# Kernel tuning notes

Measured on AMD Instinct MI355X. Metric: run time of the kernel, lower is better.

The kernel has to match this reference:

```python
import jax, jax.numpy as jnp
import numpy as np

B, M, GRID = 4, 8192, 32          # batches, points per batch, voxel grid side
N = B * M
K = 8                              # knn neighbors (includes self at dist 0)
C_IN, C_OUT, H = 8, 8, 128
KEYB = 64                          # hash base (coords shifted +1 stay in [0,33])
EPS = 1e-5


def setup_inputs() -> dict:
    rng = np.random.default_rng(0)
    # unique occupied voxels per batch (ME SparseTensor requires unique coords)
    cs = []
    for b in range(B):
        lin = rng.choice(GRID ** 3, size=M, replace=False)
        x, y, z = lin // (GRID * GRID), (lin // GRID) % GRID, lin % GRID
        cs.append(np.stack([np.full(M, b), x, y, z], axis=1))
    coords = jnp.asarray(np.concatenate(cs, axis=0).astype(np.int32))  # [N,4]

    key = jax.random.key(0)
    ks = jax.random.split(key, 4)
    feats = jax.random.normal(ks[0], (N, C_IN), jnp.float32)
    w1 = jax.random.normal(ks[1], ((K + 1) * C_IN, H), jnp.float32) * 0.05  # 1x1 conv
    g1 = jnp.ones((H,), jnp.float32)
    b1 = jnp.zeros((H,), jnp.float32)
    w3 = jax.random.normal(ks[2], (27, H, H), jnp.float32) * 0.02          # 3^3 sparse conv
    g2 = jnp.ones((H,), jnp.float32)
    b2 = jnp.zeros((H,), jnp.float32)
    w_out = jax.random.normal(ks[3], (H, 2 * C_OUT), jnp.float32) * 0.05   # 1x1 conv
    return dict(coords=coords, feats=feats, w1=w1, g1=g1, b1=b1,
                w3=w3, g2=g2, b2=b2, w_out=w_out)


def _knn_idx(coords):
    # per-batch brute-force kNN on xyz (batch column segments the search)
    xyz = coords[:, 1:].astype(jnp.float32).reshape(B, M, 3)
    d2 = jnp.sum((xyz[:, :, None, :] - xyz[:, None, :, :]) ** 2, -1)  # [B,M,M]
    _, idx = jax.lax.top_k(-d2, K)                                     # [B,M,K]
    return (idx + (jnp.arange(B) * M)[:, None, None]).reshape(N, K)


def _bn(x, g, b):
    mu = jnp.mean(x, axis=0)
    var = jnp.var(x, axis=0)
    return (x - mu) * jax.lax.rsqrt(var + EPS) * g + b


def reference(coords, feats, w1, g1, b1, w3, g2, b2, w_out):
    # --- kNN gather-and-build: [center || k neighbor feats] -> (k+1)*C_in ---
    nbr = _knn_idx(coords)                                        # [N,K] int
    combined = jnp.concatenate([feats[:, None, :], feats[nbr]], axis=1)
    combined = combined.reshape(N, (K + 1) * C_IN)
    # --- neighbor_processor: 1x1 conv + BN + ReLU ---
    h = jax.nn.relu(_bn(combined @ w1, g1, b1))                   # [N,H]
    # --- context_predictor conv k=3: gather inputs at coord+offset via hash ---
    c = coords[:, 1:] + 1                                         # shift so offsets stay >= 0
    keys = ((coords[:, 0] * KEYB + c[:, 0]) * KEYB + c[:, 1]) * KEYB + c[:, 2]
    order = jnp.argsort(keys)
    skeys = keys[order]
    offs = jnp.stack(jnp.meshgrid(*([jnp.arange(-1, 2)] * 3), indexing='ij'),
                     axis=-1).reshape(27, 3)                      # {-1,0,1}^3
    okey = (offs[:, 0] * KEYB + offs[:, 1]) * KEYB + offs[:, 2]   # [27]
    q = keys[None, :] + okey[:, None]                             # [27,N]
    pos = jnp.clip(jnp.searchsorted(skeys, q), 0, N - 1)
    valid = skeys[pos] == q                                       # [27,N]
    j = order[pos]                                                # [27,N]
    gathered = jnp.where(valid[..., None], h[j], 0.0)             # [27,N,H]
    h2 = jnp.einsum('onc,ocd->nd', gathered, w3)                  # [N,H]
    h2 = jax.nn.relu(_bn(h2, g2, b2))
    # --- final 1x1 conv -> mean/scale ---
    return h2 @ w_out                                             # [N, 2*C_OUT]
```

## Files before the change

### kernel.cpp

```cpp
#include <hip/hip_runtime.h>
#include <hip/hip_bf16.h>

#define B_   4
#define M_   8192
#define N_   32768
#define H_   128
#define EPS_ 1e-5f
#define TBL  1048576
#define GUARD 8192

typedef short short8 __attribute__((ext_vector_type(8)));
typedef float f32x4  __attribute__((ext_vector_type(4)));

__global__ __launch_bounds__(256) void prep_pack_kernel(const int* __restrict__ coords,
                                                        int* __restrict__ table,
                                                        int* __restrict__ packed,
                                                        int* __restrict__ keyb,
                                                        const float* __restrict__ w3,
                                                        ushort* __restrict__ w3f,
                                                        float* __restrict__ gsum1,
                                                        float* __restrict__ gsum2,
                                                        unsigned int* __restrict__ hbz) {
    int bid = blockIdx.x, tid = threadIdx.x;
    if (bid < 128) {
        int n = bid * 256 + tid;
        int b = coords[4*n+0], x = coords[4*n+1], y = coords[4*n+2], z = coords[4*n+3];
        packed[n] = (x << 10) | (y << 5) | z;
        int key = ((b*64 + x+1)*64 + y+1)*64 + (z+1);
        keyb[n] = key;
        table[key] = n;
        if (bid < 8)  gsum1[bid*256 + tid] = 0.f;
        if (bid == 0) gsum2[tid] = 0.f;
        if (bid == 8 && tid < 64) hbz[tid] = 0u;
        return;
    }
    int t = (bid - 128) * 256 + tid;
    int lane = t & 63;
    int ct   = (t >> 6) & 7;
    int ks   = (t >> 9) & 3;
    int o    = t >> 11;
    int quad = lane >> 4, l15 = lane & 15;
    int n = ct*16 + l15;
    const float* src = w3 + o*16384;
    ushort out8[8];
#pragma unroll
    for (int j = 0; j < 8; ++j) {
        int c = ks*32 + quad*8 + j;
        float v = src[c*128 + n];
        __hip_bfloat16 bv = __float2bfloat16(v);
        ushort u; __builtin_memcpy(&u, &bv, 2);
        out8[j] = u;
    }
    *(uint4*)&w3f[t*8] = *(uint4*)out8;
}

__global__ __launch_bounds__(256) void knn_kernel(const int* __restrict__ table,
                                                  const int* __restrict__ keyb,
                                                  const int* __restrict__ packed,
                                                  int* __restrict__ nbr) {
    __shared__ int okey_sh[96], d2_sh[96];
    __shared__ int tops[256 * 8];
    __shared__ int flagq[32];
    __shared__ int ncnt, fln;
    int tid = threadIdx.x;
    if (tid == 0) { ncnt = 0; fln = 0; }
    __syncthreads();
    if (tid < 125) {
        int dx = tid / 25 - 2, rr = tid % 25, dy = rr / 5 - 2, dz = rr % 5 - 2;
        int d2 = dx*dx + dy*dy + dz*dz;
        if (d2 <= 8) {
            int p = atomicAdd(&ncnt, 1);
            okey_sh[p] = dx * 4096 + dy * 64 + dz;
            d2_sh[p]   = d2;
        }
    }
    __syncthreads();
    if (tid < 3) { okey_sh[93 + tid] = 0; d2_sh[93 + tid] = 9; }
    __syncthreads();

    int qloc = tid >> 3;
    int q    = blockIdx.x * 32 + qloc;
    int sub  = tid & 7;
    int kb   = keyb[q];

    int top[8];
#pragma unroll
    for (int k = 0; k < 8; ++k) top[k] = 0x7FFFFFFF;

    int base = sub * 12;
    for (int i = 0; i < 12; ++i) {
        int idx = base + i;
        int j = table[kb + okey_sh[idx]];
        if (j >= 0) {
            int key = (d2_sh[idx] << 13) | (j & 8191);
            if (key < top[7]) {
#pragma unroll
                for (int k = 7; k >= 1; --k)
                    top[k] = (key < top[k]) ? max(key, top[k-1]) : top[k];
                top[0] = min(key, top[0]);
            }
        }
    }
#pragma unroll
    for (int k = 0; k < 8; ++k) tops[tid*8 + k] = top[k];
    __syncthreads();

    if (sub == 0) {
        const int* L = &tops[tid*8];
        int ia0=0, ia1=0, ia2=0, ia3=0, ia4=0, ia5=0, ia6=0, ia7=0;
        int res[8];
#pragma unroll
        for (int k = 0; k < 8; ++k) {
            int v0 = L[ia0],      v1 = L[8 + ia1],  v2 = L[16 + ia2], v3 = L[24 + ia3];
            int v4 = L[32 + ia4], v5 = L[40 + ia5], v6 = L[48 + ia6], v7 = L[56 + ia7];
            int m01 = min(v0, v1), m23 = min(v2, v3);
            int m45 = min(v4, v5), m67 = min(v6, v7);
            int m = min(min(m01, m23), min(m45, m67));
            res[k] = m;
            if      (m == v0) ++ia0; else if (m == v1) ++ia1;
            else if (m == v2) ++ia2; else if (m == v3) ++ia3;
            else if (m == v4) ++ia4; else if (m == v5) ++ia5;
            else if (m == v6) ++ia6; else ++ia7;
        }
        int bb = q & ~(M_-1);
        if ((res[7] >> 13) <= 8) {
#pragma unroll
            for (int k = 0; k < 8; ++k) nbr[q*8 + k] = bb + (res[k] & 8191);
        } else {
            int pos = atomicAdd(&fln, 1);
            flagq[pos] = q;
        }
    }
    __syncthreads();

    int fcnt = fln;
    for (int f = 0; f < fcnt; ++f) {
        int n = flagq[f];
        int bb = n & ~(M_-1);
        int p = packed[n];
        int qx = (p >> 10) & 31, qy = (p >> 5) & 31, qz = p & 31;
        int bt[8];
#pragma unroll
        for (int k = 0; k < 8; ++k) bt[k] = 0x7FFFFFFF;
        for (int j = tid; j < M_; j += 256) {
            int c = packed[bb + j];
            int dx = qx - ((c >> 10) & 31);
            int dy = qy - ((c >> 5) & 31);
            int dz = qz - (c & 31);
            int d2 = dx*dx + dy*dy + dz*dz;
            int key = (d2 << 13) | j;
            if (key < bt[7]) {
#pragma unroll
                for (int k = 7; k >= 1; --k)
                    bt[k] = (key < bt[k]) ? max(key, bt[k-1]) : bt[k];
                bt[0] = min(key, bt[0]);
            }
        }
#pragma unroll
        for (int k = 0; k < 8; ++k) tops[tid*8 + k] = bt[k];
        __syncthreads();
        for (int stride = 128; stride >= 1; stride >>= 1) {
            if (tid < stride) {
                int* A  = &tops[tid*8];
                int* Bp = &tops[(tid+stride)*8];
                int r[8]; int ia = 0, ib = 0;
#pragma unroll
                for (int k = 0; k < 8; ++k) {
                    int a = A[ia], b2 = Bp[ib];
                    if (a <= b2) { r[k] = a; ++ia; } else { r[k] = b2; ++ib; }
                }
#pragma unroll
                for (int k = 0; k < 8; ++k) A[k] = r[k];
            }
            __syncthreads();
        }
        if (tid == 0) {
#pragma unroll
            for (int k = 0; k < 8; ++k) nbr[n*8 + k] = bb + (tops[k] & 8191);
        }
        __syncthreads();
    }
}

__global__ __launch_bounds__(256) void h1_kernel(const float* __restrict__ feats,
                                                 const int* __restrict__ nbr,
                                                 const float* __restrict__ w1,
                                                 float* __restrict__ hpre,
                                                 float* __restrict__ gsum1) {
    __shared__ float comb[16][72];
    __shared__ float ssum[256], ssq[256];
    int tid = threadIdx.x;
    int rowbase = blockIdx.x * 16;
    if (tid < 144) {
        int r = tid / 9, s = tid % 9;
        int grow = rowbase + r;
        int idx = (s == 0) ? grow : nbr[grow*8 + (s-1)];
        const float4* f = (const float4*)(feats + idx * 8);
        float4 a = f[0], b = f[1];
        float* dp = &comb[r][s*8];
        dp[0]=a.x; dp[1]=a.y; dp[2]=a.z; dp[3]=a.w;
        dp[4]=b.x; dp[5]=b.y; dp[6]=b.z; dp[7]=b.w;
    }
    __syncthreads();
    int c = tid & 127, rh = tid >> 7;
    float acc[8];
#pragma unroll
    for (int i = 0; i < 8; ++i) acc[i] = 0.f;
    for (int s = 0; s < 72; ++s) {
        float w = w1[s*128 + c];
#pragma unroll
        for (int i = 0; i < 8; ++i)
            acc[i] += comb[rh*8 + i][s] * w;
    }
    float s = 0.f, q = 0.f;
#pragma unroll
    for (int i = 0; i < 8; ++i) {
        hpre[(rowbase + rh*8 + i)*128 + c] = acc[i];
        s += acc[i]; q += acc[i]*acc[i];
    }
    ssum[tid] = s; ssq[tid] = q;
    __syncthreads();
    if (tid < 128) {
        float S = ssum[tid] + ssum[tid+128];
        float Q = ssq[tid]  + ssq[tid+128];
        float* g = gsum1 + (blockIdx.x & 7) * 256;
        atomicAdd(&g[tid], S);
        atomicAdd(&g[128 + tid], Q);
    }
}

__global__ __launch_bounds__(256) void bnrelu_bf16_kernel(const float* __restrict__ x,
                                                          const float* __restrict__ gsum1,
                                                          const float* __restrict__ g1,
                                                          const float* __restrict__ b1,
                                                          ushort* __restrict__ y) {
    __shared__ float sc[128], sh[128];
    int tid = threadIdx.x;
    if (tid < 128) {
        float s = 0.f, q = 0.f;
#pragma unroll
        for (int r = 0; r < 8; ++r) {
            s += gsum1[r*256 + tid];
            q += gsum1[r*256 + 128 + tid];
        }
        float mu  = s / (float)N_;
        float var = q / (float)N_ - mu*mu;
        float inv = rsqrtf(var + EPS_);
        float scv = inv * g1[tid];
        sc[tid] = scv;
        sh[tid] = b1[tid] - mu * scv;
    }
    __syncthreads();
    int i = blockIdx.x * 256 + tid;
    float4 v = ((const float4*)x)[i];
    int c = (i * 4) & 127;
    v.x = fmaxf(0.f, v.x*sc[c]   + sh[c]);
    v.y = fmaxf(0.f, v.y*sc[c+1] + sh[c+1]);
    v.z = fmaxf(0.f, v.z*sc[c+2] + sh[c+2]);
    v.w = fmaxf(0.f, v.w*sc[c+3] + sh[c+3]);
    ushort o[4];
#pragma unroll
    for (int k = 0; k < 4; ++k) {
        float f = (&v.x)[k];
        __hip_bfloat16 bv = __float2bfloat16(f);
        __builtin_memcpy(&o[k], &bv, 2);
    }
    ((ushort4*)y)[i] = make_ushort4(o[0], o[1], o[2], o[3]);
}

#define CONV3_LDS 145408
__global__ __launch_bounds__(512) void conv3_mfma_kernel(const ushort* __restrict__ hb,
                                                         const ushort* __restrict__ w3f,
                                                         const int* __restrict__ table,
                                                         const int* __restrict__ keyb,
                                                         float* __restrict__ h2,
                                                         float* __restrict__ gsum) {
    extern __shared__ char smem_raw[];
    ushort* Asb = (ushort*)smem_raw;
    ushort* Bsb = (ushort*)(smem_raw + 65536);
    int*    jsh = (int*)(smem_raw + 131072);
    int*    kbsh= (int*)(smem_raw + 144896);

    int tid = threadIdx.x;
    int lane = tid & 63, wid = tid >> 6;
    int quad = lane >> 4, l15 = lane & 15;
    int bid = blockIdx.x;
    int swz = (bid & 7) * 32 + (bid >> 3);
    int rowbase = swz * 128;
    int wr = wid >> 1;
    int cb = (wid & 1) * 4;

    if (tid < 128) kbsh[tid] = keyb[rowbase + tid];
    __syncthreads();
    for (int t = tid; t < 27*128; t += 512) {
        int o = t >> 7, r = t & 127;
        int dx = o/9 - 1, dy = (o/3)%3 - 1, dz = o%3 - 1;
        jsh[t] = table[kbsh[r] + dx*4096 + dy*64 + dz];
    }
    __syncthreads();

#pragma unroll
    for (int i = 0; i < 4; ++i) {
        int flat = i*512 + tid;
        int r = flat >> 4, cp = flat & 15;
        int j = jsh[r];
        const ushort* asrc = hb + j*128 + ((cp ^ (r & 15)) << 3);
        __builtin_amdgcn_global_load_lds(
            (const __attribute__((address_space(1))) unsigned int*)asrc,
            (__attribute__((address_space(3))) unsigned int*)&Asb[flat << 3],
            16, 0, 0);
        __builtin_amdgcn_global_load_lds(
            (const __attribute__((address_space(1))) unsigned int*)(w3f + (flat << 3)),
            (__attribute__((address_space(3))) unsigned int*)&Bsb[flat << 3],
            16, 0, 0);
    }
    __syncthreads();

    f32x4 acc[2][4];
#pragma unroll
    for (int i = 0; i < 2; ++i)
#pragma unroll
        for (int c = 0; c < 4; ++c)
            acc[i][c] = (f32x4){0.f, 0.f, 0.f, 0.f};

    int cur = 0;
#pragma unroll 1
    for (int o = 0; o < 27; ++o) {
        if (o < 26) {
            int obase = (o + 1) << 7;
            const ushort* wsrc = w3f + ((o + 1) << 14);
            int dst = (cur ^ 1) * 16384;
#pragma unroll
            for (int i = 0; i < 4; ++i) {
                int flat = i*512 + tid;
                int r = flat >> 4, cp = flat & 15;
                int j = jsh[obase + r];
                const ushort* asrc = hb + j*128 + ((cp ^ (r & 15)) << 3);
                __builtin_amdgcn_global_load_lds(
                    (const __attribute__((address_space(1))) unsigned int*)asrc,
                    (__attribute__((address_space(3))) unsigned int*)&Asb[dst + (flat << 3)],
                    16, 0, 0);
                __builtin_amdgcn_global_load_lds(
                    (const __attribute__((address_space(1))) unsigned int*)(wsrc + (flat << 3)),
                    (__attribute__((address_space(3))) unsigned int*)&Bsb[dst + (flat << 3)],
                    16, 0, 0);
            }
        }
        const ushort* Ac = Asb + cur*16384;
        const ushort* Bc = Bsb + cur*16384;
#pragma unroll
        for (int ks = 0; ks < 4; ++ks) {
            short8 af[2], bfr[4];
#pragma unroll
            for (int i = 0; i < 2; ++i) {
                int lr = wr*32 + i*16 + l15;
                int chunk = (ks*4 + quad) ^ l15;
                af[i] = *(const short8*)&Ac[lr*128 + chunk*8];
            }
#pragma unroll
            for (int c = 0; c < 4; ++c)
                bfr[c] = *(const short8*)&Bc[((ks*8 + cb + c)*64 + lane) << 3];
#pragma unroll
            for (int i = 0; i < 2; ++i)
#pragma unroll
                for (int c = 0; c < 4; ++c)
                    acc[i][c] = __builtin_amdgcn_mfma_f32_16x16x32_bf16(af[i], bfr[c], acc[i][c], 0, 0, 0);
        }
        __syncthreads();
        cur ^= 1;
    }

    float s[4], q[4];
#pragma unroll
    for (int c = 0; c < 4; ++c) { s[c] = 0.f; q[c] = 0.f; }
#pragma unroll
    for (int i = 0; i < 2; ++i)
#pragma unroll
        for (int c = 0; c < 4; ++c)
#pragma unroll
            for (int r = 0; r < 4; ++r) {
                int row = rowbase + wr*32 + i*16 + quad*4 + r;
                int col = (cb + c)*16 + l15;
                float v = acc[i][c][r];
                h2[row*128 + col] = v;
                s[c] += v; q[c] += v*v;
            }
    float* red = (float*)smem_raw;
    if (tid < 256) red[tid] = 0.f;
    __syncthreads();
#pragma unroll
    for (int c = 0; c < 4; ++c) {
        int col = (cb + c)*16 + l15;
        atomicAdd(&red[col], s[c]);
        atomicAdd(&red[128 + col], q[c]);
    }
    __syncthreads();
    if (tid < 256) atomicAdd(&gsum[tid], red[tid]);
}

__global__ __launch_bounds__(256) void out_kernel(const float* __restrict__ h2,
                                                  const float* __restrict__ wout,
                                                  const float* __restrict__ gsum2,
                                                  const float* __restrict__ g2,
                                                  const float* __restrict__ b2,
                                                  float* __restrict__ out) {
    __shared__ float hrow[128][129];
    __shared__ float wsh[2048];
    __shared__ float sc[128], sh[128];
    int tid = threadIdx.x;
    if (tid < 128) {
        float s = gsum2[tid], q = gsum2[128 + tid];
        float mu  = s / (float)N_;
        float var = q / (float)N_ - mu*mu;
        float inv = rsqrtf(var + EPS_);
        float scv = inv * g2[tid];
        sc[tid] = scv;
        sh[tid] = b2[tid] - mu * scv;
    }
#pragma unroll
    for (int i = 0; i < 8; ++i) wsh[i*256 + tid] = wout[i*256 + tid];
    __syncthreads();

    int rowbase = blockIdx.x * 128;
#pragma unroll
    for (int i = 0; i < 16; ++i) {
        int flat = i*256 + tid;
        int row = flat >> 5, c4 = (flat & 31) * 4;
        float4 v = *(const float4*)&h2[(rowbase + row)*128 + c4];
        float4 scv = *(const float4*)&sc[c4];
        float4 shv = *(const float4*)&sh[c4];
        hrow[row][c4+0] = fmaxf(0.f, fmaf(v.x, scv.x, shv.x));
        hrow[row][c4+1] = fmaxf(0.f, fmaf(v.y, scv.y, shv.y));
        hrow[row][c4+2] = fmaxf(0.f, fmaf(v.z, scv.z, shv.z));
        hrow[row][c4+3] = fmaxf(0.f, fmaf(v.w, scv.w, shv.w));
    }
    __syncthreads();

    int row = tid >> 1, dbase = (tid & 1) * 8;
    float acc[8];
#pragma unroll
    for (int k = 0; k < 8; ++k) acc[k] = 0.f;
    for (int c = 0; c < 128; ++c) {
        float hv = hrow[row][c];
        float4 w0 = *(const float4*)&wsh[c*16 + dbase];
        float4 w1 = *(const float4*)&wsh[c*16 + dbase + 4];
        acc[0] = fmaf(hv, w0.x, acc[0]);
        acc[1] = fmaf(hv, w0.y, acc[1]);
        acc[2] = fmaf(hv, w0.z, acc[2]);
        acc[3] = fmaf(hv, w0.w, acc[3]);
        acc[4] = fmaf(hv, w1.x, acc[4]);
        acc[5] = fmaf(hv, w1.y, acc[5]);
        acc[6] = fmaf(hv, w1.z, acc[6]);
        acc[7] = fmaf(hv, w1.w, acc[7]);
    }
    float* op = out + (rowbase + row)*16 + dbase;
    *(float4*)op       = (float4){acc[0], acc[1], acc[2], acc[3]};
    *(float4*)(op + 4) = (float4){acc[4], acc[5], acc[6], acc[7]};
}

extern "C" void kernel_launch(void* const* d_in, const int* in_sizes, int n_in,
                              void* d_out, int out_size, void* d_ws, size_t ws_size,
                              hipStream_t stream) {
    const int*   coords = (const int*)d_in[0];
    const float* feats  = (const float*)d_in[1];
    const float* w1     = (const float*)d_in[2];
    const float* g1     = (const float*)d_in[3];
    const float* b1     = (const float*)d_in[4];
    const float* w3     = (const float*)d_in[5];
    const float* g2     = (const float*)d_in[6];
    const float* b2     = (const float*)d_in[7];
    const float* wout   = (const float*)d_in[8];
    float* out = (float*)d_out;

    char* ws = (char*)d_ws;
    int*    table_base = (int*)(ws);
    int*    table   = table_base + GUARD;
    int*    packed  = (int*)(ws + (4352u<<10));
    int*    keyb    = (int*)(ws + (4608u<<10));
    int*    nbr     = (int*)(ws + (4864u<<10));
    float*  gsum2   = (float*)(ws + (6416u<<10));
    float*  gsum1   = (float*)(ws + (6420u<<10));
    ushort* w3f     = (ushort*)(ws + (6656u<<10));
    ushort* hb      = (ushort*)(ws + (7680u<<10));
    float*  h       = (float*)(ws + (15872u<<10));
    float*  h2      = h;

    static bool conv3_attr_set = false;
    if (!conv3_attr_set) {
        hipFuncSetAttribute(reinterpret_cast<const void*>(&conv3_mfma_kernel),
                            hipFuncAttributeMaxDynamicSharedMemorySize, CONV3_LDS);
        conv3_attr_set = true;
    }

    hipMemsetAsync(table_base, 0xFF, (TBL + GUARD) * sizeof(int), stream);
    prep_pack_kernel <<<344, 256, 0, stream>>>(coords, table, packed, keyb, w3, w3f,
                                               gsum1, gsum2, (unsigned int*)(hb - 128));
    knn_kernel       <<<N_/32, 256, 0, stream>>>(table, keyb, packed, nbr);
    h1_kernel        <<<N_/16, 256, 0, stream>>>(feats, nbr, w1, h, gsum1);
    bnrelu_bf16_kernel<<<(N_*H_/4)/256, 256, 0, stream>>>(h, gsum1, g1, b1, hb);
    conv3_mfma_kernel<<<N_/128, 512, CONV3_LDS, stream>>>(hb, w3f, table, keyb, h2, gsum2);
    out_kernel       <<<N_/128, 256, 0, stream>>>(h2, wout, gsum2, g2, b2, out);
}
```

Before: 213.9 us.

## Assign one wavefront per kNN query with shuffle-based top-8 selection

The kNN kernel now maps each query to a full 64-lane wavefront. Each lane probes one or two of the 93 hash offsets, and the 8 smallest keys are picked by repeated wave-wide xor-shuffle min reductions. This replaces the per-thread insertion sort, the LDS staging and the serial 8-way merge. The grid grows from N/32 to N/4 blocks, and each block still pays the offset-table setup and still reserves the 8 KB tops array for the rare brute-force fallback, which may limit occupancy.

```diff
diff --git a/kernel.cpp b/kernel.cpp
--- a/kernel.cpp
+++ b/kernel.cpp
@@ -58,9 +58,9 @@
                                                   const int* __restrict__ keyb,
                                                   const int* __restrict__ packed,
                                                   int* __restrict__ nbr) {
-    __shared__ int okey_sh[96], d2_sh[96];
+    __shared__ int okey_sh[93], d2_sh[93];
     __shared__ int tops[256 * 8];
-    __shared__ int flagq[32];
+    __shared__ int flagq[4];
     __shared__ int ncnt, fln;
     int tid = threadIdx.x;
     if (tid == 0) { ncnt = 0; fln = 0; }
@@ -75,54 +75,37 @@
         }
     }
     __syncthreads();
-    if (tid < 3) { okey_sh[93 + tid] = 0; d2_sh[93 + tid] = 9; }
-    __syncthreads();
-
-    int qloc = tid >> 3;
-    int q    = blockIdx.x * 32 + qloc;
-    int sub  = tid & 7;
-    int kb   = keyb[q];
-
-    int top[8];
-#pragma unroll
-    for (int k = 0; k < 8; ++k) top[k] = 0x7FFFFFFF;
-
-    int base = sub * 12;
-    for (int i = 0; i < 12; ++i) {
-        int idx = base + i;
-        int j = table[kb + okey_sh[idx]];
-        if (j >= 0) {
-            int key = (d2_sh[idx] << 13) | (j & 8191);
-            if (key < top[7]) {
-#pragma unroll
-                for (int k = 7; k >= 1; --k)
-                    top[k] = (key < top[k]) ? max(key, top[k-1]) : top[k];
-                top[0] = min(key, top[0]);
-            }
-        }
-    }
-#pragma unroll
-    for (int k = 0; k < 8; ++k) tops[tid*8 + k] = top[k];
-    __syncthreads();
-
-    if (sub == 0) {
-        const int* L = &tops[tid*8];
-        int ia0=0, ia1=0, ia2=0, ia3=0, ia4=0, ia5=0, ia6=0, ia7=0;
-        int res[8];
-#pragma unroll
-        for (int k = 0; k < 8; ++k) {
-            int v0 = L[ia0],      v1 = L[8 + ia1],  v2 = L[16 + ia2], v3 = L[24 + ia3];
-            int v4 = L[32 + ia4], v5 = L[40 + ia5], v6 = L[48 + ia6], v7 = L[56 + ia7];
-            int m01 = min(v0, v1), m23 = min(v2, v3);
-            int m45 = min(v4, v5), m67 = min(v6, v7);
-            int m = min(min(m01, m23), min(m45, m67));
-            res[k] = m;
-            if      (m == v0) ++ia0; else if (m == v1) ++ia1;
-            else if (m == v2) ++ia2; else if (m == v3) ++ia3;
-            else if (m == v4) ++ia4; else if (m == v5) ++ia5;
-            else if (m == v6) ++ia6; else ++ia7;
-        }
-        int bb = q & ~(M_-1);
+
+    int lane = tid & 63, wv = tid >> 6;
+    int q  = blockIdx.x * 4 + wv;
+    int kb = keyb[q];
+    int bb = q & ~(M_-1);
+
+    int k0 = 0x40000000 | (lane << 1);
+    int k1 = 0x40000000 | (lane << 1) | 1;
+    {
+        int j0 = table[kb + okey_sh[lane]];
+        if (j0 >= 0) k0 = (d2_sh[lane] << 13) | (j0 & 8191);
+    }
+    if (lane < 29) {
+        int c1 = 64 + lane;
+        int j1 = table[kb + okey_sh[c1]];
+        if (j1 >= 0) k1 = (d2_sh[c1] << 13) | (j1 & 8191);
+    }
+
+    int res[8];
+#pragma unroll
+    for (int k = 0; k < 8; ++k) {
+        int m = min(k0, k1);
+#pragma unroll
+        for (int d = 1; d < 64; d <<= 1)
+            m = min(m, __shfl_xor(m, d));
+        res[k] = m;
+        if (k0 == m) k0 = 0x7FFFFFFF;
+        else if (k1 == m) k1 = 0x7FFFFFFF;
+    }
+
+    if (lane == 0) {
         if ((res[7] >> 13) <= 8) {
 #pragma unroll
             for (int k = 0; k < 8; ++k) nbr[q*8 + k] = bb + (res[k] & 8191);
@@ -136,14 +119,14 @@
     int fcnt = fln;
     for (int f = 0; f < fcnt; ++f) {
         int n = flagq[f];
-        int bb = n & ~(M_-1);
+        int nbb = n & ~(M_-1);
         int p = packed[n];
         int qx = (p >> 10) & 31, qy = (p >> 5) & 31, qz = p & 31;
         int bt[8];
 #pragma unroll
         for (int k = 0; k < 8; ++k) bt[k] = 0x7FFFFFFF;
         for (int j = tid; j < M_; j += 256) {
-            int c = packed[bb + j];
+            int c = packed[nbb + j];
             int dx = qx - ((c >> 10) & 31);
             int dy = qy - ((c >> 5) & 31);
             int dz = qz - (c & 31);
@@ -176,7 +159,7 @@
         }
         if (tid == 0) {
 #pragma unroll
-            for (int k = 0; k < 8; ++k) nbr[n*8 + k] = bb + (tops[k] & 8191);
+            for (int k = 0; k < 8; ++k) nbr[n*8 + k] = nbb + (tops[k] & 8191);
         }
         __syncthreads();
     }
@@ -495,7 +478,7 @@
     hipMemsetAsync(table_base, 0xFF, (TBL + GUARD) * sizeof(int), stream);
     prep_pack_kernel <<<344, 256, 0, stream>>>(coords, table, packed, keyb, w3, w3f,
                                                gsum1, gsum2, (unsigned int*)(hb - 128));
-    knn_kernel       <<<N_/32, 256, 0, stream>>>(table, keyb, packed, nbr);
+    knn_kernel       <<<N_/4, 256, 0, stream>>>(table, keyb, packed, nbr);
     h1_kernel        <<<N_/16, 256, 0, stream>>>(feats, nbr, w1, h, gsum1);
     bnrelu_bf16_kernel<<<(N_*H_/4)/256, 256, 0, stream>>>(h, gsum1, g1, b1, hb);
     conv3_mfma_kernel<<<N_/128, 512, CONV3_LDS, stream>>>(hb, w3f, table, keyb, h2, gsum2);
```

Measured after the change: 195.2 us. 8.8% less time.
